# Kernel tuning notes

Measured on AMD Instinct MI355X. Metric: run time of the kernel, lower is better.

The kernel has to match this reference:

```python
import jax, jax.numpy as jnp
import numpy as np

NEG_INF = -1e30


def setup_inputs() -> dict:
    key = jax.random.key(0)
    k1, k2, k3, k4 = jax.random.split(key, 4)
    B, T, C, H = 4, 4096, 1024, 64
    x = jax.random.normal(k1, (B, T, C), dtype=jnp.float32)
    Wk = jax.random.normal(k2, (C, H), dtype=jnp.float32) * (C ** -0.5)
    Wq = jax.random.normal(k3, (C, H), dtype=jnp.float32) * (C ** -0.5)
    Wv = jax.random.normal(k4, (C, H), dtype=jnp.float32) * (C ** -0.5)
    return {"x": x, "Wk": Wk, "Wq": Wq, "Wv": Wv}


def reference(x, Wk, Wq, Wv):
    # x: [B, T, C]; Wq/Wk/Wv: [C, H]
    B, T, C = x.shape
    q = jnp.einsum('btc,ch->bth', x, Wq)  # [B,T,H]
    k = jnp.einsum('btc,ch->bth', x, Wk)  # [B,T,H]
    v = jnp.einsum('btc,ch->bth', x, Wv)  # [B,T,H]
    # NOTE: original scales by C**-0.5 (n_embd), not head_size**-0.5.
    scale = jnp.asarray(C, x.dtype) ** -0.5
    wei = jnp.einsum('bth,bsh->bts', q, k) * scale  # [B,T,T]
    causal = jnp.tril(jnp.ones((T, T), dtype=bool))
    wei = jnp.where(causal, wei, NEG_INF)
    wei = jax.nn.softmax(wei, axis=-1)
    # dropout p=0.0 -> identity
    out = jnp.einsum('bts,bsh->bth', wei, v)  # [B,T,H]
    return out
```

## Files before the change

### kernel.cpp

```cpp
#include <hip/hip_runtime.h>
#include <math.h>

typedef short bfx8 __attribute__((ext_vector_type(8)));
typedef short bfx4 __attribute__((ext_vector_type(4)));
typedef float fx4  __attribute__((ext_vector_type(4)));
typedef unsigned int ux2 __attribute__((ext_vector_type(2)));
typedef unsigned int ux4v __attribute__((ext_vector_type(4)));

__device__ __forceinline__ unsigned short f2bf(float f) {
    unsigned int u = __builtin_bit_cast(unsigned int, f);
    u += 0x7FFFu + ((u >> 16) & 1u);
    return (unsigned short)(u >> 16);
}
__device__ __forceinline__ float bf2f(unsigned short s) {
    unsigned int u = ((unsigned int)s) << 16;
    return __builtin_bit_cast(float, u);
}
__device__ __forceinline__ unsigned int cvtpk(float a, float b) {
    unsigned int d;
    asm("v_cvt_pk_bf16_f32 %0, %1, %2" : "=v"(d) : "v"(a), "v"(b));
    return d;
}

__global__ __launch_bounds__(256) void wt_prep(const float* __restrict__ Wq,
                                               const float* __restrict__ Wk,
                                               const float* __restrict__ Wv,
                                               unsigned short* __restrict__ wt)
{
    const int k0  = blockIdx.x * 64;
    const int mat = blockIdx.y;
    const float* W = (mat == 0) ? Wq : ((mat == 1) ? Wk : Wv);
    const float scale = (mat == 0) ? (0.03125f * 1.4426950408889634f) : 1.0f;
    __shared__ unsigned short Ls[64 * 68];
    const int t = threadIdx.x;
    #pragma unroll
    for (int i = 0; i < 4; ++i) {
        int idx4 = t + 256 * i;
        int r = idx4 >> 4, c4 = idx4 & 15;
        float4 v = *(const float4*)&W[(size_t)(k0 + r) * 64 + c4 * 4];
        Ls[r * 68 + c4 * 4 + 0] = f2bf(v.x * scale);
        Ls[r * 68 + c4 * 4 + 1] = f2bf(v.y * scale);
        Ls[r * 68 + c4 * 4 + 2] = f2bf(v.z * scale);
        Ls[r * 68 + c4 * 4 + 3] = f2bf(v.w * scale);
    }
    __syncthreads();
    #pragma unroll
    for (int i = 0; i < 2; ++i) {
        int u = t + 256 * i;
        int n = u >> 3, kc = u & 7;
        bfx8 o;
        #pragma unroll
        for (int j = 0; j < 8; ++j) o[j] = (short)Ls[(kc * 8 + j) * 68 + n];
        *(bfx8*)&wt[(size_t)(mat * 64 + n) * 1024 + k0 + kc * 8] = o;
    }
}

__global__ __launch_bounds__(256) void qkv_mfma(
    const float* __restrict__ x, const unsigned short* __restrict__ wt,
    unsigned short* __restrict__ qb, unsigned short* __restrict__ kb,
    unsigned short* __restrict__ vt)
{
    __shared__ alignas(16) char smem[57344];
    const int t = threadIdx.x;
    const int w = t >> 6, l = t & 63, g = l >> 4, li = l & 15;
    const int m0 = blockIdx.x * 32;
    const int rh  = (w & 1) * 16;
    const int nb0 = (w >> 1) * 6;

    fx4 acc[6];
    #pragma unroll
    for (int i = 0; i < 6; ++i) acc[i] = (fx4){0.f, 0.f, 0.f, 0.f};

    float4 xr[2];

    const unsigned short* wSrc[6];
    #pragma unroll
    for (int i = 0; i < 6; ++i) {
        int s = w * 6144 + i * 1024 + l * 16;
        int n = s >> 7, c = ((s >> 4) & 7) ^ (n & 7);
        wSrc[i] = wt + (size_t)n * 1024 + c * 8;
    }

#define QKV_DMA_W(K0, BI) do { \
    _Pragma("unroll") for (int i_ = 0; i_ < 6; ++i_) \
        __builtin_amdgcn_global_load_lds( \
            (const __attribute__((address_space(1))) void*)(wSrc[i_] + (K0)), \
            (__attribute__((address_space(3))) void*)(smem + 8192 + (BI) * 24576 + w * 6144 + i_ * 1024), \
            16, 0, 0); \
} while (0)

#define QKV_LOAD_X(K0) do { \
    _Pragma("unroll") for (int i_ = 0; i_ < 2; ++i_) { int idx4 = t + 256 * i_; int r_ = idx4 >> 4, c4 = idx4 & 15; \
        xr[i_] = *(const float4*)&x[(size_t)(m0 + r_) * 1024 + (K0) + c4 * 4]; } \
} while (0)

#define QKV_STORE_X(BI) do { \
    char* xb_ = smem + (BI) * 4096; \
    _Pragma("unroll") for (int i_ = 0; i_ < 2; ++i_) { int idx4 = t + 256 * i_; int r_ = idx4 >> 4, c4 = idx4 & 15; \
        ux2 u_; u_[0] = cvtpk(xr[i_].x, xr[i_].y); u_[1] = cvtpk(xr[i_].z, xr[i_].w); \
        *(ux2*)(xb_ + ((r_ * 128 + c4 * 8) ^ ((r_ & 7) << 4))) = u_; } \
} while (0)

    QKV_LOAD_X(0); QKV_STORE_X(0); QKV_DMA_W(0, 0);
    __syncthreads();

    for (int ch = 0; ch < 16; ++ch) {
        if (ch + 1 < 16) { QKV_DMA_W((ch + 1) * 64, (ch + 1) & 1); QKV_LOAD_X((ch + 1) * 64); }
        char* xb = smem + (ch & 1) * 4096;
        char* wb = smem + 8192 + (ch & 1) * 24576;
        const int arow = rh + li;
        #pragma unroll
        for (int kk = 0; kk < 2; ++kk) {
            bfx8 af = *(bfx8*)(xb + ((arow * 128 + kk * 64 + g * 16) ^ ((arow & 7) << 4)));
            #pragma unroll
            for (int nb = 0; nb < 6; ++nb) {
                int nrow = (nb0 + nb) * 16 + li;
                bfx8 bf = *(bfx8*)(wb + ((nrow * 128 + kk * 64 + g * 16) ^ ((nrow & 7) << 4)));
                acc[nb] = __builtin_amdgcn_mfma_f32_16x16x32_bf16(af, bf, acc[nb], 0, 0, 0);
            }
        }
        if (ch + 1 < 16) QKV_STORE_X((ch + 1) & 1);
        __syncthreads();
    }

    const int mrow = m0 + rh + g * 4;
    #pragma unroll
    for (int nb = 0; nb < 6; ++nb) {
        const int nbg = nb0 + nb;
        if (nbg < 4) {
            #pragma unroll
            for (int r = 0; r < 4; ++r)
                qb[(size_t)(mrow + r) * 64 + nbg * 16 + li] = f2bf(acc[nb][r]);
        } else if (nbg < 8) {
            #pragma unroll
            for (int r = 0; r < 4; ++r)
                kb[(size_t)(mrow + r) * 64 + (nbg - 4) * 16 + li] = f2bf(acc[nb][r]);
        }
    }

    __syncthreads();
    unsigned short* Vt = (unsigned short*)smem;
    #pragma unroll
    for (int nb = 0; nb < 6; ++nb) {
        const int nbg = nb0 + nb;
        if (nbg >= 8) {
            #pragma unroll
            for (int r = 0; r < 4; ++r)
                Vt[((nbg - 8) * 16 + li) * 40 + g * 8 + (rh >> 2) + r] = f2bf(acc[nb][r]);
        }
    }
    __syncthreads();
    const int bb = m0 >> 12, mt = m0 & 4095;
    {
        int d = t >> 2, c = t & 3;
        *(bfx8*)&vt[((size_t)(bb * 64 + d)) * 4096 + mt + c * 8] = *(bfx8*)&Vt[d * 40 + c * 8];
    }
}

__global__ __launch_bounds__(256, 4) void attn_mfma(
    const unsigned short* __restrict__ qb, const unsigned short* __restrict__ kb,
    const unsigned short* __restrict__ vt,
    unsigned short* __restrict__ pO, float* __restrict__ pml)
{
    __shared__ alignas(16) char smem[34816];
    const int t = threadIdx.x;
    const int w = t >> 6, l = t & 63, g = l >> 4, li = l & 15;
    const int bx = blockIdx.x;

    const int b = bx & 3;
    const int j = bx >> 2;
    int qt, seg, nch;
    if (j < 224) {
        int a = 1;
        #pragma unroll
        for (int aa = 2; aa <= 7; ++aa) if (j >= 4 * aa * (aa - 1)) a = aa;
        const int local = j - 4 * a * (a - 1);
        qt = 8 * a + local / a;
        seg = local % a;
        nch = 8;
    } else {
        const int jd = j - 224;
        const int r = 7 - (jd >> 3);
        const int a = jd & 7;
        qt = 8 * a + r; seg = a; nch = r + 1;
    }
    const int qbase = qt * 64;
    const int kvb = seg * 512;
    const int qsub = w & 1, par = w >> 1;
    const int qmax_w = qbase + qsub * 32 + 31;
    const int aq = qt >> 3, rq = qt & 7;
    const int slot = b * 288 + (aq + 1) * (4 * aq + rq) + seg;

    const unsigned short* Qg = qb + (size_t)b * 4096 * 64;
    const unsigned short* Kg = kb + (size_t)b * 4096 * 64;
    const unsigned short* Vg = vt + (size_t)b * 64 * 4096;

    const unsigned short* kSrc[2];
    const unsigned short* vSrc[2];
    #pragma unroll
    for (int i = 0; i < 2; ++i) {
        int s = w * 2048 + i * 1024 + l * 16;
        int r = s >> 7, c = ((s >> 4) & 7) ^ (r & 7);
        kSrc[i] = Kg + (size_t)r * 64 + c * 8;
        vSrc[i] = Vg + (size_t)r * 4096 + c * 8;
    }

#define ATT_DMA(CB, BI) do { \
    _Pragma("unroll") for (int i_ = 0; i_ < 2; ++i_) { \
        __builtin_amdgcn_global_load_lds( \
            (const __attribute__((address_space(1))) void*)(kSrc[i_] + (size_t)(CB) * 64), \
            (__attribute__((address_space(3))) void*)(smem + (BI) * 8192 + w * 2048 + i_ * 1024), 16, 0, 0); \
        __builtin_amdgcn_global_load_lds( \
            (const __attribute__((address_space(1))) void*)(vSrc[i_] + (CB)), \
            (__attribute__((address_space(3))) void*)(smem + 16384 + (BI) * 8192 + w * 2048 + i_ * 1024), 16, 0, 0); } \
} while (0)

    bfx8 qf[2][2];
    #pragma unroll
    for (int f = 0; f < 2; ++f)
        #pragma unroll
        for (int h = 0; h < 2; ++h)
            qf[f][h] = *(const bfx8*)&Qg[(size_t)(qbase + qsub * 32 + f * 16 + li) * 64 + h * 32 + g * 8];

    ATT_DMA(kvb, 0);
    if (nch > 1) ATT_DMA(kvb + 64, 1);

    fx4 o[4][2];
    #pragma unroll
    for (int i = 0; i < 4; ++i)
        #pragma unroll
        for (int f = 0; f < 2; ++f) o[i][f] = (fx4){0.f, 0.f, 0.f, 0.f};
    float lsum[2] = {0.f, 0.f};

    for (int ch = 0; ch < nch; ++ch) {
        if (ch < nch - 1) { asm volatile("s_waitcnt vmcnt(4)" ::: "memory"); }
        else              { asm volatile("s_waitcnt vmcnt(0)" ::: "memory"); }
        __builtin_amdgcn_sched_barrier(0);
        __builtin_amdgcn_s_barrier();
        asm volatile("" ::: "memory");

        char* ks = smem + (ch & 1) * 8192;
        char* vs = smem + 16384 + (ch & 1) * 8192;
        const int cb = kvb + (ch << 6);
        const int sub = cb + par * 32;
        if (sub <= qmax_w) {
            fx4 s[2][2];
            #pragma unroll
            for (int st = 0; st < 2; ++st)
                #pragma unroll
                for (int f = 0; f < 2; ++f) s[st][f] = (fx4){0.f, 0.f, 0.f, 0.f};
            __builtin_amdgcn_s_setprio(1);
            #pragma unroll
            for (int st = 0; st < 2; ++st) {
                const int krow = par * 32 + st * 16 + li;
                const int sw = (krow & 7) << 4;
                bfx8 kf0 = *(bfx8*)(ks + ((krow * 128 + g * 16) ^ sw));
                bfx8 kf1 = *(bfx8*)(ks + ((krow * 128 + 64 + g * 16) ^ sw));
                #pragma unroll
                for (int f = 0; f < 2; ++f) {
                    s[st][f] = __builtin_amdgcn_mfma_f32_16x16x32_bf16(kf0, qf[f][0], s[st][f], 0, 0, 0);
                    s[st][f] = __builtin_amdgcn_mfma_f32_16x16x32_bf16(kf1, qf[f][1], s[st][f], 0, 0, 0);
                }
            }
            __builtin_amdgcn_s_setprio(0);

            bfx8 pf[2];
            #pragma unroll
            for (int f = 0; f < 2; ++f) {
                const int qmin_f = qbase + qsub * 32 + f * 16;
                float p[8];
                if (sub + 31 > qmin_f) {
                    #pragma unroll
                    for (int st = 0; st < 2; ++st)
                        #pragma unroll
                        for (int rr = 0; rr < 4; ++rr) {
                            int kv = sub + st * 16 + 4 * g + rr;
                            p[st * 4 + rr] = (kv <= qmin_f + li) ? s[st][f][rr] : -1e30f;
                        }
                } else {
                    #pragma unroll
                    for (int st = 0; st < 2; ++st)
                        #pragma unroll
                        for (int rr = 0; rr < 4; ++rr) p[st * 4 + rr] = s[st][f][rr];
                }
                #pragma unroll
                for (int e = 0; e < 8; ++e) p[e] = exp2f(p[e]);
                lsum[f] += ((p[0]+p[1])+(p[2]+p[3])) + ((p[4]+p[5])+(p[6]+p[7]));
                ux4v pu;
                pu[0] = cvtpk(p[0], p[1]); pu[1] = cvtpk(p[2], p[3]);
                pu[2] = cvtpk(p[4], p[5]); pu[3] = cvtpk(p[6], p[7]);
                pf[f] = __builtin_bit_cast(bfx8, pu);
            }

            __builtin_amdgcn_s_setprio(1);
            #pragma unroll
            for (int dblk = 0; dblk < 4; ++dblk) {
                const int dr = dblk * 16 + li;
                bfx8 vf = *(bfx8*)(vs + ((dr * 128 + par * 64 + g * 16) ^ ((dr & 7) << 4)));
                #pragma unroll
                for (int f = 0; f < 2; ++f)
                    o[dblk][f] = __builtin_amdgcn_mfma_f32_16x16x32_bf16(vf, pf[f], o[dblk][f], 0, 0, 0);
            }
            __builtin_amdgcn_s_setprio(0);
        }

        __builtin_amdgcn_s_barrier();
        asm volatile("" ::: "memory");
        if (ch + 2 < nch) ATT_DMA(kvb + ((ch + 2) << 6), ch & 1);
    }
    asm volatile("" ::: "memory");

    float* Osh = (float*)smem;
    float* lsh = (float*)(smem + 32768);
    #pragma unroll
    for (int dblk = 0; dblk < 4; ++dblk)
        #pragma unroll
        for (int f = 0; f < 2; ++f)
            #pragma unroll
            for (int r = 0; r < 4; ++r)
                Osh[(par * 64 + qsub * 32 + f * 16 + li) * 64 + dblk * 16 + g * 4 + r] = o[dblk][f][r];
    #pragma unroll
    for (int f = 0; f < 2; ++f)
        lsh[((w * 2 + f) * 4 + g) * 16 + li] = lsum[f];
    __syncthreads();

    {
        const int q = t >> 2, dg = t & 3;
        const int A = (q >> 5), Bw = A + 2, fq = (q >> 4) & 1, liq = q & 15;
        float L = 0.f;
        #pragma unroll
        for (int gg2 = 0; gg2 < 4; ++gg2)
            L += lsh[((A * 2 + fq) * 4 + gg2) * 16 + liq] + lsh[((Bw * 2 + fq) * 4 + gg2) * 16 + liq];
        const float* OA = &Osh[q * 64 + dg * 16];
        const float* OB = &Osh[(64 + q) * 64 + dg * 16];
        ux4v u1, u2;
        u1[0] = cvtpk(OA[0] + OB[0],  OA[1] + OB[1]);
        u1[1] = cvtpk(OA[2] + OB[2],  OA[3] + OB[3]);
        u1[2] = cvtpk(OA[4] + OB[4],  OA[5] + OB[5]);
        u1[3] = cvtpk(OA[6] + OB[6],  OA[7] + OB[7]);
        u2[0] = cvtpk(OA[8] + OB[8],  OA[9] + OB[9]);
        u2[1] = cvtpk(OA[10] + OB[10], OA[11] + OB[11]);
        u2[2] = cvtpk(OA[12] + OB[12], OA[13] + OB[13]);
        u2[3] = cvtpk(OA[14] + OB[14], OA[15] + OB[15]);
        unsigned short* dst = pO + (size_t)slot * 4096 + q * 64 + dg * 16;
        *(bfx8*)&dst[0] = __builtin_bit_cast(bfx8, u1);
        *(bfx8*)&dst[8] = __builtin_bit_cast(bfx8, u2);
        if (dg == 0) pml[(size_t)slot * 64 + q] = L;
    }
}

__global__ __launch_bounds__(256) void attn_merge(
    const unsigned short* __restrict__ pO, const float* __restrict__ pml,
    float* __restrict__ out)
{
    const int b = blockIdx.x & 3, qt = blockIdx.x >> 2;
    const int a = qt >> 3, r = qt & 7;
    const int nseg = a + 1;
    const int slot0 = b * 288 + (a + 1) * (4 * a + r);
    const int t = threadIdx.x;
    const int q = t >> 2, dg = t & 3;

    float L = 0.f;
    float acc[16];
    #pragma unroll
    for (int jj = 0; jj < 16; ++jj) acc[jj] = 0.f;
    #pragma unroll
    for (int s = 0; s < 8; ++s) {
        if (s < nseg) {
            L += pml[(size_t)(slot0 + s) * 64 + q];
            const unsigned short* src = pO + (size_t)(slot0 + s) * 4096 + q * 64 + dg * 16;
            bfx8 v0 = *(const bfx8*)&src[0];
            bfx8 v1 = *(const bfx8*)&src[8];
            #pragma unroll
            for (int jj = 0; jj < 8; ++jj) acc[jj]     += bf2f((unsigned short)v0[jj]);
            #pragma unroll
            for (int jj = 0; jj < 8; ++jj) acc[8 + jj] += bf2f((unsigned short)v1[jj]);
        }
    }
    const float inv = 1.f / L;
    float* orow = out + ((size_t)b * 4096 + qt * 64 + q) * 64 + dg * 16;
    #pragma unroll
    for (int v4 = 0; v4 < 4; ++v4) {
        float4 rr;
        rr.x = acc[v4 * 4 + 0] * inv; rr.y = acc[v4 * 4 + 1] * inv;
        rr.z = acc[v4 * 4 + 2] * inv; rr.w = acc[v4 * 4 + 3] * inv;
        *(float4*)&orow[v4 * 4] = rr;
    }
}

extern "C" void kernel_launch(void* const* d_in, const int* in_sizes, int n_in,
                              void* d_out, int out_size, void* d_ws, size_t ws_size,
                              hipStream_t stream)
{
    const float* x  = (const float*)d_in[0];
    const float* Wk = (const float*)d_in[1];
    const float* Wq = (const float*)d_in[2];
    const float* Wv = (const float*)d_in[3];
    float* outp = (float*)d_out;

    char* ws = (char*)d_ws;
    unsigned short* qbuf = (unsigned short*)(ws);
    unsigned short* kbuf = (unsigned short*)(ws + 2*1024*1024);
    unsigned short* vtb  = (unsigned short*)(ws + 4*1024*1024);
    unsigned short* wtb  = (unsigned short*)(ws + 6*1024*1024);
    unsigned short* pO   = (unsigned short*)(ws + 7*1024*1024);
    float*          pml  = (float*)(ws + 16*1024*1024 + 512*1024);

    wt_prep<<<dim3(16, 3), 256, 0, stream>>>(Wq, Wk, Wv, wtb);
    qkv_mfma<<<512, 256, 0, stream>>>(x, wtb, qbuf, kbuf, vtb);
    attn_mfma<<<1152, 256, 0, stream>>>(qbuf, kbuf, vtb, pO, pml);
    attn_merge<<<256, 256, 0, stream>>>(pO, pml, outp);
}
```

Measured before the change: 56.28 us.

## Split attention KV range into 256-key segments for finer work decomposition

Changes the split-KV decomposition of the causal attention kernel from 512-key segments (8 chunks) to 256-key segments (4 chunks), raising the grid from 1152 to 2176 blocks. Slot indexing for partial outputs and the merge kernel are updated to match, and the merge loop now runs over a dynamic segment count. Smaller segments shorten the longest blocks and improve load balance across CUs. The cost is more partial-output traffic and more merge work. Swizzled LDS offsets are also precomputed outside the chunk loop.

```diff
diff --git a/kernel.cpp b/kernel.cpp
--- a/kernel.cpp
+++ b/kernel.cpp
@@ -167,29 +167,31 @@
     const int w = t >> 6, l = t & 63, g = l >> 4, li = l & 15;
     const int bx = blockIdx.x;
 
-    const int b = bx & 3;
-    const int j = bx >> 2;
-    int qt, seg, nch;
-    if (j < 224) {
-        int a = 1;
-        #pragma unroll
-        for (int aa = 2; aa <= 7; ++aa) if (j >= 4 * aa * (aa - 1)) a = aa;
-        const int local = j - 4 * a * (a - 1);
-        qt = 8 * a + local / a;
-        seg = local % a;
-        nch = 8;
+    int b, qt, s4, nch;
+    if (bx < 1984) {
+        b = bx & 3;
+        int fj = bx >> 2;
+        int acc2 = 0; qt = 3; s4 = 0;
+        for (int qq = 3; qq < 64; ++qq) {
+            int fl = (qq + 1) >> 2;
+            if (fj < acc2 + fl) { qt = qq; s4 = fj - acc2; break; }
+            acc2 += fl;
+        }
+        nch = 4;
     } else {
-        const int jd = j - 224;
-        const int r = 7 - (jd >> 3);
-        const int a = jd & 7;
-        qt = 8 * a + r; seg = a; nch = r + 1;
+        int r2 = bx - 1984; b = r2 & 3;
+        int j2 = r2 >> 2;
+        int grp = j2 >> 4, idx = j2 & 15;
+        qt = idx * 4 + (2 - grp);
+        s4 = (qt + 1) >> 2;
+        nch = (qt + 1) & 3;
     }
     const int qbase = qt * 64;
-    const int kvb = seg * 512;
+    const int kvb = s4 * 256;
     const int qsub = w & 1, par = w >> 1;
     const int qmax_w = qbase + qsub * 32 + 31;
-    const int aq = qt >> 3, rq = qt & 7;
-    const int slot = b * 288 + (aq + 1) * (4 * aq + rq) + seg;
+    const int aa = qt >> 2, rr = qt & 3;
+    const int slot = b * 544 + (aa + 1) * (2 * aa + rr) + s4;
 
     const unsigned short* Qg = qb + (size_t)b * 4096 * 64;
     const unsigned short* Kg = kb + (size_t)b * 4096 * 64;
@@ -222,6 +224,20 @@
         for (int h = 0; h < 2; ++h)
             qf[f][h] = *(const bfx8*)&Qg[(size_t)(qbase + qsub * 32 + f * 16 + li) * 64 + h * 32 + g * 8];
 
+    int kOffB[2][2], vOffB[4];
+    #pragma unroll
+    for (int st = 0; st < 2; ++st) {
+        const int krow = par * 32 + st * 16 + li;
+        const int sw = (krow & 7) << 4;
+        kOffB[st][0] = krow * 128 + ((g * 16) ^ sw);
+        kOffB[st][1] = krow * 128 + ((64 + g * 16) ^ sw);
+    }
+    #pragma unroll
+    for (int dblk = 0; dblk < 4; ++dblk) {
+        const int dr = dblk * 16 + li;
+        vOffB[dblk] = dr * 128 + ((par * 64 + g * 16) ^ ((dr & 7) << 4));
+    }
+
     ATT_DMA(kvb, 0);
     if (nch > 1) ATT_DMA(kvb + 64, 1);
 
@@ -252,10 +268,8 @@
             __builtin_amdgcn_s_setprio(1);
             #pragma unroll
             for (int st = 0; st < 2; ++st) {
-                const int krow = par * 32 + st * 16 + li;
-                const int sw = (krow & 7) << 4;
-                bfx8 kf0 = *(bfx8*)(ks + ((krow * 128 + g * 16) ^ sw));
-                bfx8 kf1 = *(bfx8*)(ks + ((krow * 128 + 64 + g * 16) ^ sw));
+                bfx8 kf0 = *(bfx8*)(ks + kOffB[st][0]);
+                bfx8 kf1 = *(bfx8*)(ks + kOffB[st][1]);
                 #pragma unroll
                 for (int f = 0; f < 2; ++f) {
                     s[st][f] = __builtin_amdgcn_mfma_f32_16x16x32_bf16(kf0, qf[f][0], s[st][f], 0, 0, 0);
@@ -273,15 +287,15 @@
                     #pragma unroll
                     for (int st = 0; st < 2; ++st)
                         #pragma unroll
-                        for (int rr = 0; rr < 4; ++rr) {
-                            int kv = sub + st * 16 + 4 * g + rr;
-                            p[st * 4 + rr] = (kv <= qmin_f + li) ? s[st][f][rr] : -1e30f;
+                        for (int rr2 = 0; rr2 < 4; ++rr2) {
+                            int kv = sub + st * 16 + 4 * g + rr2;
+                            p[st * 4 + rr2] = (kv <= qmin_f + li) ? s[st][f][rr2] : -1e30f;
                         }
                 } else {
                     #pragma unroll
                     for (int st = 0; st < 2; ++st)
                         #pragma unroll
-                        for (int rr = 0; rr < 4; ++rr) p[st * 4 + rr] = s[st][f][rr];
+                        for (int rr2 = 0; rr2 < 4; ++rr2) p[st * 4 + rr2] = s[st][f][rr2];
                 }
                 #pragma unroll
                 for (int e = 0; e < 8; ++e) p[e] = exp2f(p[e]);
@@ -295,8 +309,7 @@
             __builtin_amdgcn_s_setprio(1);
             #pragma unroll
             for (int dblk = 0; dblk < 4; ++dblk) {
-                const int dr = dblk * 16 + li;
-                bfx8 vf = *(bfx8*)(vs + ((dr * 128 + par * 64 + g * 16) ^ ((dr & 7) << 4)));
+                bfx8 vf = *(bfx8*)(vs + vOffB[dblk]);
                 #pragma unroll
                 for (int f = 0; f < 2; ++f)
                     o[dblk][f] = __builtin_amdgcn_mfma_f32_16x16x32_bf16(vf, pf[f], o[dblk][f], 0, 0, 0);
@@ -354,9 +367,9 @@
     float* __restrict__ out)
 {
     const int b = blockIdx.x & 3, qt = blockIdx.x >> 2;
-    const int a = qt >> 3, r = qt & 7;
-    const int nseg = a + 1;
-    const int slot0 = b * 288 + (a + 1) * (4 * a + r);
+    const int aa = qt >> 2, rr = qt & 3;
+    const int nseg = (qt + 4) >> 2;
+    const int slot0 = b * 544 + (aa + 1) * (2 * aa + rr);
     const int t = threadIdx.x;
     const int q = t >> 2, dg = t & 3;
 
@@ -364,27 +377,24 @@
     float acc[16];
     #pragma unroll
     for (int jj = 0; jj < 16; ++jj) acc[jj] = 0.f;
-    #pragma unroll
-    for (int s = 0; s < 8; ++s) {
-        if (s < nseg) {
-            L += pml[(size_t)(slot0 + s) * 64 + q];
-            const unsigned short* src = pO + (size_t)(slot0 + s) * 4096 + q * 64 + dg * 16;
-            bfx8 v0 = *(const bfx8*)&src[0];
-            bfx8 v1 = *(const bfx8*)&src[8];
-            #pragma unroll
-            for (int jj = 0; jj < 8; ++jj) acc[jj]     += bf2f((unsigned short)v0[jj]);
-            #pragma unroll
-            for (int jj = 0; jj < 8; ++jj) acc[8 + jj] += bf2f((unsigned short)v1[jj]);
-        }
+    for (int s = 0; s < nseg; ++s) {
+        L += pml[(size_t)(slot0 + s) * 64 + q];
+        const unsigned short* src = pO + (size_t)(slot0 + s) * 4096 + q * 64 + dg * 16;
+        bfx8 v0 = *(const bfx8*)&src[0];
+        bfx8 v1 = *(const bfx8*)&src[8];
+        #pragma unroll
+        for (int jj = 0; jj < 8; ++jj) acc[jj]     += bf2f((unsigned short)v0[jj]);
+        #pragma unroll
+        for (int jj = 0; jj < 8; ++jj) acc[8 + jj] += bf2f((unsigned short)v1[jj]);
     }
     const float inv = 1.f / L;
     float* orow = out + ((size_t)b * 4096 + qt * 64 + q) * 64 + dg * 16;
     #pragma unroll
     for (int v4 = 0; v4 < 4; ++v4) {
-        float4 rr;
-        rr.x = acc[v4 * 4 + 0] * inv; rr.y = acc[v4 * 4 + 1] * inv;
-        rr.z = acc[v4 * 4 + 2] * inv; rr.w = acc[v4 * 4 + 3] * inv;
-        *(float4*)&orow[v4 * 4] = rr;
+        float4 rv;
+        rv.x = acc[v4 * 4 + 0] * inv; rv.y = acc[v4 * 4 + 1] * inv;
+        rv.z = acc[v4 * 4 + 2] * inv; rv.w = acc[v4 * 4 + 3] * inv;
+        *(float4*)&orow[v4 * 4] = rv;
     }
 }
 
@@ -404,10 +414,10 @@
     unsigned short* vtb  = (unsigned short*)(ws + 4*1024*1024);
     unsigned short* wtb  = (unsigned short*)(ws + 6*1024*1024);
     unsigned short* pO   = (unsigned short*)(ws + 7*1024*1024);
-    float*          pml  = (float*)(ws + 16*1024*1024 + 512*1024);
+    float*          pml  = (float*)(ws + 25*1024*1024);
 
     wt_prep<<<dim3(16, 3), 256, 0, stream>>>(Wq, Wk, Wv, wtb);
     qkv_mfma<<<512, 256, 0, stream>>>(x, wtb, qbuf, kbuf, vtb);
-    attn_mfma<<<1152, 256, 0, stream>>>(qbuf, kbuf, vtb, pO, pml);
+    attn_mfma<<<2176, 256, 0, stream>>>(qbuf, kbuf, vtb, pO, pml);
     attn_merge<<<256, 256, 0, stream>>>(pO, pml, outp);
 }
```

Measured after the change: 62.99 us. +11.9%, slower.

## Enlarge attention query tile to 128 rows with 512-thread blocks

Applied to the files above, without the earlier changes.

The attention kernel now handles 128 query rows per block with 8 waves instead of 64 rows with 4 waves. Each K/V chunk loaded into shared memory is therefore reused by twice as many queries, and each wave issues one DMA per tensor instead of two. The work-split schedule, partial-output slots and the merge kernel are all rewritten for the larger tile, and the cross-wave reduction now accumulates in shared memory. The cost is fewer blocks (576), so per-CU parallelism is coarser and causal load balance may be worse.

```diff
diff --git a/kernel.cpp b/kernel.cpp
--- a/kernel.cpp
+++ b/kernel.cpp
@@ -157,12 +157,12 @@
     }
 }
 
-__global__ __launch_bounds__(256, 4) void attn_mfma(
+__global__ __launch_bounds__(512, 4) void attn_mfma(
     const unsigned short* __restrict__ qb, const unsigned short* __restrict__ kb,
     const unsigned short* __restrict__ vt,
     unsigned short* __restrict__ pO, float* __restrict__ pml)
 {
-    __shared__ alignas(16) char smem[34816];
+    __shared__ alignas(16) char smem[36864];
     const int t = threadIdx.x;
     const int w = t >> 6, l = t & 63, g = l >> 4, li = l & 15;
     const int bx = blockIdx.x;
@@ -170,49 +170,51 @@
     const int b = bx & 3;
     const int j = bx >> 2;
     int qt, seg, nch;
-    if (j < 224) {
-        int a = 1;
-        #pragma unroll
-        for (int aa = 2; aa <= 7; ++aa) if (j >= 4 * aa * (aa - 1)) a = aa;
-        const int local = j - 4 * a * (a - 1);
-        qt = 8 * a + local / a;
-        seg = local % a;
-        nch = 8;
+    if (j < 120) {
+        int a = 0;
+        #pragma unroll
+        for (int aa = 1; aa <= 7; ++aa) if (j >= aa * (2 * aa - 1)) a = aa;
+        const int local = j - a * (2 * a - 1);
+        int r;
+        if      (local <     a) { r = 0; seg = local; }
+        else if (local < 2 * a) { r = 1; seg = local - a; }
+        else if (local < 3 * a) { r = 2; seg = local - 2 * a; }
+        else                    { r = 3; seg = local - 3 * a; }
+        qt = 4 * a + r; nch = 8;
     } else {
-        const int jd = j - 224;
-        const int r = 7 - (jd >> 3);
-        const int a = jd & 7;
-        qt = 8 * a + r; seg = a; nch = r + 1;
-    }
-    const int qbase = qt * 64;
+        const int jd = j - 120;
+        const int grp = jd >> 3, a = jd & 7;
+        const int r = 2 - grp;
+        qt = 4 * a + r; seg = a; nch = 2 * r + 2;
+    }
+    const int qbase = qt * 128;
     const int kvb = seg * 512;
-    const int qsub = w & 1, par = w >> 1;
+    const int qsub = w & 3, par = w >> 2;
     const int qmax_w = qbase + qsub * 32 + 31;
-    const int aq = qt >> 3, rq = qt & 7;
-    const int slot = b * 288 + (aq + 1) * (4 * aq + rq) + seg;
+    const int a2 = qt >> 2, r2 = qt & 3;
+    const int slot = b * 144 + (a2 + 1) * (2 * a2 + r2) + seg;
 
     const unsigned short* Qg = qb + (size_t)b * 4096 * 64;
     const unsigned short* Kg = kb + (size_t)b * 4096 * 64;
     const unsigned short* Vg = vt + (size_t)b * 64 * 4096;
 
-    const unsigned short* kSrc[2];
-    const unsigned short* vSrc[2];
-    #pragma unroll
-    for (int i = 0; i < 2; ++i) {
-        int s = w * 2048 + i * 1024 + l * 16;
-        int r = s >> 7, c = ((s >> 4) & 7) ^ (r & 7);
-        kSrc[i] = Kg + (size_t)r * 64 + c * 8;
-        vSrc[i] = Vg + (size_t)r * 4096 + c * 8;
+    const unsigned short* kSrc;
+    const unsigned short* vSrc;
+    {
+        int ofs = w * 1024 + l * 16;
+        int row = ofs >> 7, sl = (ofs >> 4) & 7;
+        int c = sl ^ (row & 7);
+        kSrc = Kg + (size_t)row * 64 + c * 8;
+        vSrc = Vg + (size_t)row * 4096 + c * 8;
     }
 
 #define ATT_DMA(CB, BI) do { \
-    _Pragma("unroll") for (int i_ = 0; i_ < 2; ++i_) { \
-        __builtin_amdgcn_global_load_lds( \
-            (const __attribute__((address_space(1))) void*)(kSrc[i_] + (size_t)(CB) * 64), \
-            (__attribute__((address_space(3))) void*)(smem + (BI) * 8192 + w * 2048 + i_ * 1024), 16, 0, 0); \
-        __builtin_amdgcn_global_load_lds( \
-            (const __attribute__((address_space(1))) void*)(vSrc[i_] + (CB)), \
-            (__attribute__((address_space(3))) void*)(smem + 16384 + (BI) * 8192 + w * 2048 + i_ * 1024), 16, 0, 0); } \
+    __builtin_amdgcn_global_load_lds( \
+        (const __attribute__((address_space(1))) void*)(kSrc + (size_t)(CB) * 64), \
+        (__attribute__((address_space(3))) void*)(smem + (BI) * 8192 + w * 1024), 16, 0, 0); \
+    __builtin_amdgcn_global_load_lds( \
+        (const __attribute__((address_space(1))) void*)(vSrc + (CB)), \
+        (__attribute__((address_space(3))) void*)(smem + 16384 + (BI) * 8192 + w * 1024), 16, 0, 0); \
 } while (0)
 
     bfx8 qf[2][2];
@@ -233,7 +235,7 @@
     float lsum[2] = {0.f, 0.f};
 
     for (int ch = 0; ch < nch; ++ch) {
-        if (ch < nch - 1) { asm volatile("s_waitcnt vmcnt(4)" ::: "memory"); }
+        if (ch < nch - 1) { asm volatile("s_waitcnt vmcnt(2)" ::: "memory"); }
         else              { asm volatile("s_waitcnt vmcnt(0)" ::: "memory"); }
         __builtin_amdgcn_sched_barrier(0);
         __builtin_amdgcn_s_barrier();
@@ -313,39 +315,50 @@
     float* Osh = (float*)smem;
     float* lsh = (float*)(smem + 32768);
     #pragma unroll
-    for (int dblk = 0; dblk < 4; ++dblk)
-        #pragma unroll
-        for (int f = 0; f < 2; ++f)
-            #pragma unroll
-            for (int r = 0; r < 4; ++r)
-                Osh[(par * 64 + qsub * 32 + f * 16 + li) * 64 + dblk * 16 + g * 4 + r] = o[dblk][f][r];
-    #pragma unroll
     for (int f = 0; f < 2; ++f)
         lsh[((w * 2 + f) * 4 + g) * 16 + li] = lsum[f];
-    __syncthreads();
-
-    {
-        const int q = t >> 2, dg = t & 3;
-        const int A = (q >> 5), Bw = A + 2, fq = (q >> 4) & 1, liq = q & 15;
-        float L = 0.f;
-        #pragma unroll
-        for (int gg2 = 0; gg2 < 4; ++gg2)
-            L += lsh[((A * 2 + fq) * 4 + gg2) * 16 + liq] + lsh[((Bw * 2 + fq) * 4 + gg2) * 16 + liq];
-        const float* OA = &Osh[q * 64 + dg * 16];
-        const float* OB = &Osh[(64 + q) * 64 + dg * 16];
-        ux4v u1, u2;
-        u1[0] = cvtpk(OA[0] + OB[0],  OA[1] + OB[1]);
-        u1[1] = cvtpk(OA[2] + OB[2],  OA[3] + OB[3]);
-        u1[2] = cvtpk(OA[4] + OB[4],  OA[5] + OB[5]);
-        u1[3] = cvtpk(OA[6] + OB[6],  OA[7] + OB[7]);
-        u2[0] = cvtpk(OA[8] + OB[8],  OA[9] + OB[9]);
-        u2[1] = cvtpk(OA[10] + OB[10], OA[11] + OB[11]);
-        u2[2] = cvtpk(OA[12] + OB[12], OA[13] + OB[13]);
-        u2[3] = cvtpk(OA[14] + OB[14], OA[15] + OB[15]);
-        unsigned short* dst = pO + (size_t)slot * 4096 + q * 64 + dg * 16;
-        *(bfx8*)&dst[0] = __builtin_bit_cast(bfx8, u1);
-        *(bfx8*)&dst[8] = __builtin_bit_cast(bfx8, u2);
-        if (dg == 0) pml[(size_t)slot * 64 + q] = L;
+    if (par == 1) {
+        #pragma unroll
+        for (int dblk = 0; dblk < 4; ++dblk)
+            #pragma unroll
+            for (int f = 0; f < 2; ++f)
+                #pragma unroll
+                for (int r = 0; r < 4; ++r)
+                    Osh[(qsub * 32 + f * 16 + li) * 64 + dblk * 16 + g * 4 + r] = o[dblk][f][r];
+    }
+    __syncthreads();
+
+    if (par == 0) {
+        #pragma unroll
+        for (int f = 0; f < 2; ++f) {
+            const int qrow = qsub * 32 + f * 16 + li;
+            #pragma unroll
+            for (int dblk = 0; dblk < 4; ++dblk)
+                #pragma unroll
+                for (int r = 0; r < 4; ++r)
+                    Osh[qrow * 64 + dblk * 16 + g * 4 + r] += o[dblk][f][r];
+            if (g == 0) {
+                float L = 0.f;
+                #pragma unroll
+                for (int p2 = 0; p2 < 2; ++p2)
+                    #pragma unroll
+                    for (int gg = 0; gg < 4; ++gg)
+                        L += lsh[(((p2 * 4 + qsub) * 2 + f) * 4 + gg) * 16 + li];
+                pml[(size_t)slot * 128 + qrow] = L;
+            }
+        }
+    }
+    __syncthreads();
+
+    #pragma unroll
+    for (int i = 0; i < 2; ++i) {
+        int u = t + 512 * i;
+        int q = u >> 3, c = u & 7;
+        const float* src = &Osh[q * 64 + c * 8];
+        ux4v uo;
+        uo[0] = cvtpk(src[0], src[1]); uo[1] = cvtpk(src[2], src[3]);
+        uo[2] = cvtpk(src[4], src[5]); uo[3] = cvtpk(src[6], src[7]);
+        *(bfx8*)&pO[(size_t)slot * 8192 + q * 64 + c * 8] = __builtin_bit_cast(bfx8, uo);
     }
 }
 
@@ -354,37 +367,34 @@
     float* __restrict__ out)
 {
     const int b = blockIdx.x & 3, qt = blockIdx.x >> 2;
-    const int a = qt >> 3, r = qt & 7;
+    const int a = qt >> 2, r = qt & 3;
     const int nseg = a + 1;
-    const int slot0 = b * 288 + (a + 1) * (4 * a + r);
+    const int slot0 = b * 144 + (a + 1) * (2 * a + r);
     const int t = threadIdx.x;
-    const int q = t >> 2, dg = t & 3;
+    const int q = t >> 1, d0 = (t & 1) * 32;
 
     float L = 0.f;
-    float acc[16];
-    #pragma unroll
-    for (int jj = 0; jj < 16; ++jj) acc[jj] = 0.f;
-    #pragma unroll
-    for (int s = 0; s < 8; ++s) {
-        if (s < nseg) {
-            L += pml[(size_t)(slot0 + s) * 64 + q];
-            const unsigned short* src = pO + (size_t)(slot0 + s) * 4096 + q * 64 + dg * 16;
-            bfx8 v0 = *(const bfx8*)&src[0];
-            bfx8 v1 = *(const bfx8*)&src[8];
-            #pragma unroll
-            for (int jj = 0; jj < 8; ++jj) acc[jj]     += bf2f((unsigned short)v0[jj]);
-            #pragma unroll
-            for (int jj = 0; jj < 8; ++jj) acc[8 + jj] += bf2f((unsigned short)v1[jj]);
+    float acc[32];
+    #pragma unroll
+    for (int jj = 0; jj < 32; ++jj) acc[jj] = 0.f;
+    for (int s = 0; s < nseg; ++s) {
+        L += pml[(size_t)(slot0 + s) * 128 + q];
+        const unsigned short* src = pO + (size_t)(slot0 + s) * 8192 + q * 64 + d0;
+        #pragma unroll
+        for (int v = 0; v < 4; ++v) {
+            bfx8 vv = *(const bfx8*)&src[v * 8];
+            #pragma unroll
+            for (int jj = 0; jj < 8; ++jj) acc[v * 8 + jj] += bf2f((unsigned short)vv[jj]);
         }
     }
     const float inv = 1.f / L;
-    float* orow = out + ((size_t)b * 4096 + qt * 64 + q) * 64 + dg * 16;
-    #pragma unroll
-    for (int v4 = 0; v4 < 4; ++v4) {
-        float4 rr;
-        rr.x = acc[v4 * 4 + 0] * inv; rr.y = acc[v4 * 4 + 1] * inv;
-        rr.z = acc[v4 * 4 + 2] * inv; rr.w = acc[v4 * 4 + 3] * inv;
-        *(float4*)&orow[v4 * 4] = rr;
+    float* orow = out + ((size_t)b * 4096 + qt * 128 + q) * 64 + d0;
+    #pragma unroll
+    for (int v4 = 0; v4 < 8; ++v4) {
+        float4 rv;
+        rv.x = acc[v4 * 4 + 0] * inv; rv.y = acc[v4 * 4 + 1] * inv;
+        rv.z = acc[v4 * 4 + 2] * inv; rv.w = acc[v4 * 4 + 3] * inv;
+        *(float4*)&orow[v4 * 4] = rv;
     }
 }
 
@@ -404,10 +414,10 @@
     unsigned short* vtb  = (unsigned short*)(ws + 4*1024*1024);
     unsigned short* wtb  = (unsigned short*)(ws + 6*1024*1024);
     unsigned short* pO   = (unsigned short*)(ws + 7*1024*1024);
-    float*          pml  = (float*)(ws + 16*1024*1024 + 512*1024);
+    float*          pml  = (float*)(ws + 17*1024*1024);
 
     wt_prep<<<dim3(16, 3), 256, 0, stream>>>(Wq, Wk, Wv, wtb);
     qkv_mfma<<<512, 256, 0, stream>>>(x, wtb, qbuf, kbuf, vtb);
-    attn_mfma<<<1152, 256, 0, stream>>>(qbuf, kbuf, vtb, pO, pml);
-    attn_merge<<<256, 256, 0, stream>>>(pO, pml, outp);
-}
+    attn_mfma<<<576, 512, 0, stream>>>(qbuf, kbuf, vtb, pO, pml);
+    attn_merge<<<128, 256, 0, stream>>>(pO, pml, outp);
+}
```

Result: slower. 60.78 us (+8.0%).
